# Kernel tuning notes

Measured on AMD Instinct MI355X. Metric: run time of the kernel, lower is better.

## Reference

```python
import jax, jax.numpy as jnp
import numpy as np
from jax.ops import segment_sum

N_NODES = 100000
N_EDGES = 3200000
DIM = 256
N_CLASSES = 32
N_GRAPHS = 64


def setup_inputs() -> dict:
    key = jax.random.key(0)
    k1, k2, k3, k4, k5 = jax.random.split(key, 5)
    x = jax.random.normal(k1, (N_NODES, DIM), dtype=jnp.float32)
    W = jax.random.normal(k2, (DIM, N_CLASSES), dtype=jnp.float32) / np.sqrt(DIM)
    b = jax.random.normal(k3, (N_CLASSES,), dtype=jnp.float32) * 0.01
    edge_index = jax.random.randint(k4, (2, N_EDGES), 0, N_NODES, dtype=jnp.int64)
    batch = jnp.sort(jax.random.randint(k5, (N_NODES,), 0, N_GRAPHS, dtype=jnp.int64))
    return {"x": x, "W": W, "b": b, "edge_index": edge_index, "batch": batch}


def reference(x, W, b, edge_index, batch):
    N = x.shape[0]
    # GCNConv: linear transform (no bias), then normalized aggregation, then bias
    h = x @ W  # [N, C]
    # add self loops (PyG default add_self_loops=True)
    loop = jnp.arange(N, dtype=edge_index.dtype)
    src = jnp.concatenate([edge_index[0], loop])  # source (message sender)
    dst = jnp.concatenate([edge_index[1], loop])  # target (aggregation site)
    # symmetric normalization: deg computed at target with unit edge weights
    deg = segment_sum(jnp.ones_like(dst, dtype=h.dtype), dst, num_segments=N)
    dinv = jnp.where(deg > 0, jax.lax.rsqrt(deg), 0.0)
    norm = dinv[src] * dinv[dst]  # [E+N]
    msg = h[src] * norm[:, None]  # gather + scale
    out = segment_sum(msg, dst, num_segments=N) + b  # scatter-add, bias after agg
    # global_mean_pool: segment mean over graphs
    cnt = segment_sum(jnp.ones((N,), dtype=out.dtype), batch, num_segments=N_GRAPHS)
    sums = segment_sum(out, batch, num_segments=N_GRAPHS)
    return sums / jnp.maximum(cnt, 1.0)[:, None]
```

## Files before the change

kernel.cpp:

```cpp
#include <hip/hip_runtime.h>

#define NN    100000
#define NE    3200000
#define DIMK  256
#define NC    32
#define NG    64

#define ROWS   64
#define NBUCK  1563
#define CAP    2432
#define NB1    512
#define EPB    6250
#define NSL    16
#define MAXG   512

static constexpr size_t OFF_REC    = 0;
static constexpr size_t OFF_DINV   = 15204864;
static constexpr size_t OFF_BTOT   = 15604864;
static constexpr size_t OFF_START  = 15613056;
static constexpr size_t OFF_CTRL   = 15613568;
static constexpr size_t OFF_P2     = 15613696;
static constexpr size_t OFF_PART   = 16662272;
static constexpr size_t OFF_NODEI  = OFF_PART;
static constexpr size_t OFF_CNT    = OFF_PART + 400000;
static constexpr size_t OFF_EXC    = OFF_PART + 3601024;

__device__ __forceinline__ int idx_at(const void* p, long i, bool i64) {
    return i64 ? (int)((const long long*)p)[i] : ((const int*)p)[i];
}

__device__ __forceinline__ bool detect_i64(const void* ei) {
    const int* w = (const int*)ei;
    return (w[1] == 0) & (w[3] == 0) & (w[5] == 0) &
           (w[7] == 0) & (w[9] == 0) & (w[11] == 0);
}

__global__ __launch_bounds__(256) void k_pre(const void* __restrict__ ei,
        unsigned int* __restrict__ parts, int* __restrict__ cnt) {
    __shared__ unsigned int h[12500];
    const bool i64 = detect_i64(ei);
    const int b = blockIdx.x;
    if (b < 256) {
        const int hh = b >> 7;
        const int sl = b & 127;
        const int lo = hh * 50000, hi = lo + 50000;
        for (int t = threadIdx.x; t < 12500; t += 256) h[t] = 0u;
        __syncthreads();
        const int e0 = sl * 25000;
        for (int e = e0 + threadIdx.x; e < e0 + 25000; e += 256) {
            int d = idx_at(ei, (long)NE + e, i64);
            if (d >= lo && d < hi) {
                int r = d - lo;
                atomicAdd(&h[r >> 2], 1u << ((r & 3) * 8));
            }
        }
        __syncthreads();
        for (int t = threadIdx.x; t < 12500; t += 256)
            parts[(size_t)b * 12500 + t] = h[t];
    } else {
        const int k = b - 256;
        for (int t = threadIdx.x; t < NBUCK; t += 256) h[t] = 0u;
        __syncthreads();
        const int e0 = k * EPB;
        for (int e = e0 + threadIdx.x; e < e0 + EPB; e += 256) {
            int s = idx_at(ei, e, i64);
            atomicAdd(&h[s >> 6], 1u);
        }
        __syncthreads();
        for (int t = threadIdx.x; t < NBUCK; t += 256)
            cnt[t * NB1 + k] = (int)h[t];
    }
}

__global__ __launch_bounds__(512) void k_mid(const unsigned int* __restrict__ parts,
        unsigned int* __restrict__ nodeinfo, float* __restrict__ dinv,
        const void* __restrict__ batch, const void* __restrict__ ei,
        int* __restrict__ start, const int* __restrict__ cnt,
        int* __restrict__ exc, int* __restrict__ btot) {
    __shared__ int s[512];
    const int b = blockIdx.x;
    const int t = threadIdx.x;
    if (b < 49) {
        const bool i64 = detect_i64(ei);
        int i = b * 512 + t;
        if (i >= 25000) return;
        int h = (i >= 12500) ? 1 : 0;
        int w = i - h * 12500;
        int c0 = 0, c1 = 0, c2 = 0, c3 = 0;
        const unsigned int* base = parts + (size_t)(h * 128) * 12500 + w;
#pragma unroll 4
        for (int q = 0; q < 128; ++q) {
            unsigned int v = base[(size_t)q * 12500];
            c0 += v & 255u; c1 += (v >> 8) & 255u; c2 += (v >> 16) & 255u; c3 += v >> 24;
        }
        int node = h * 50000 + w * 4;
        dinv[node]     = 1.0f / sqrtf((float)(1 + c0));
        dinv[node + 1] = 1.0f / sqrtf((float)(1 + c1));
        dinv[node + 2] = 1.0f / sqrtf((float)(1 + c2));
        dinv[node + 3] = 1.0f / sqrtf((float)(1 + c3));
        nodeinfo[node]     = ((unsigned)(1 + c0) << 6) | (unsigned)idx_at(batch, node, i64);
        nodeinfo[node + 1] = ((unsigned)(1 + c1) << 6) | (unsigned)idx_at(batch, node + 1, i64);
        nodeinfo[node + 2] = ((unsigned)(1 + c2) << 6) | (unsigned)idx_at(batch, node + 2, i64);
        nodeinfo[node + 3] = ((unsigned)(1 + c3) << 6) | (unsigned)idx_at(batch, node + 3, i64);
    } else if (b < 245) {
        const bool i64 = detect_i64(ei);
        int i = (b - 49) * 512 + t;
        if (i >= NN) return;
        int bi = idx_at(batch, i, i64);
        int bp = (i == 0) ? -1 : idx_at(batch, i - 1, i64);
        for (int g = bp + 1; g <= bi; ++g) start[g] = i;
        if (i == NN - 1)
            for (int g = bi + 1; g <= NG; ++g) start[g] = NN;
    } else {
        const int bkt = b - 245;
        int v = cnt[bkt * NB1 + t];
        s[t] = v;
        __syncthreads();
        for (int off = 1; off < 512; off <<= 1) {
            int u = (t >= off) ? s[t - off] : 0;
            __syncthreads();
            s[t] += u;
            __syncthreads();
        }
        exc[bkt * NB1 + t] = bkt * CAP + (s[t] - v);
        if (t == 511) btot[bkt] = s[511];
    }
}

__global__ __launch_bounds__(256) void k_place(const void* __restrict__ ei,
        const unsigned int* __restrict__ nodeinfo,
        const int* __restrict__ exc, unsigned int* __restrict__ rec,
        int* __restrict__ ctrl) {
    __shared__ unsigned int lc[NBUCK];
    __shared__ int lbase[NBUCK];
    const bool i64 = detect_i64(ei);
    const int k = blockIdx.x;
    if (k == 0 && threadIdx.x == 0) ctrl[1] = 0;
    for (int t = threadIdx.x; t < NBUCK; t += 256) {
        lc[t] = 0u;
        lbase[t] = exc[t * NB1 + k];
    }
    __syncthreads();
    const int e0 = k * EPB;
    for (int e = e0 + threadIdx.x; e < e0 + EPB; e += 256) {
        int s = idx_at(ei, e, i64);
        int d = idx_at(ei, (long)NE + e, i64);
        unsigned int ni = nodeinfo[d];
        unsigned int deg = min(ni >> 6, 1048575u);
        unsigned int g = ni & 63u;
        int b = s >> 6;
        unsigned int r = atomicAdd(&lc[b], 1u);
        rec[lbase[b] + (int)r] = (deg << 12) | (g * 64 + (unsigned)(s & 63));
    }
}

__global__ __launch_bounds__(512, 2) void k_fused(
        const float* __restrict__ x, const float* __restrict__ dinv,
        const void* __restrict__ batch, const void* __restrict__ ei,
        const unsigned int* __restrict__ rec, const int* __restrict__ btot,
        float* __restrict__ part, int* __restrict__ ctrl) {
    __shared__ __align__(16) float Ach[64 * ROWS];
    __shared__ int sbkt;
    const bool i64 = detect_i64(ei);
    const int tid  = threadIdx.x;
    const int gi   = tid >> 6;
    const int lane = tid & 63;

    float acc[8][4];
#pragma unroll
    for (int g = 0; g < 8; ++g)
#pragma unroll
        for (int d = 0; d < 4; ++d) acc[g][d] = 0.0f;

    const float4* x4 = (const float4*)x;
    float4* Ach4 = (float4*)Ach;
    const float4 z4 = make_float4(0.f, 0.f, 0.f, 0.f);
    const int jmax = NN - 1;

    for (;;) {
        if (tid == 0) sbkt = atomicAdd(&ctrl[1], 1);
        __syncthreads();
        const int bkt = sbkt;
        if (bkt >= NBUCK) break;
        const int j0 = bkt * ROWS;

        Ach4[tid] = z4;
        Ach4[tid + 512] = z4;
        __syncthreads();
        if (tid < ROWS) {
            int j = j0 + tid;
            if (j < NN) Ach[idx_at(batch, j, i64) * 64 + tid] = dinv[j];
        }
        __syncthreads();
        {
            const int rb = bkt * CAP;
            const int re = rb + btot[bkt];
            for (int r = rb + tid; r < re; r += 512) {
                unsigned int q = rec[r];
                float val = 1.0f / sqrtf((float)(q >> 12));
                atomicAdd(&Ach[q & 4095u], val);
            }
        }
        __syncthreads();
        float areg[8];
        {
            float dv = dinv[min(j0 + lane, jmax)];
#pragma unroll
            for (int q = 0; q < 8; ++q)
                areg[q] = Ach[(gi * 8 + q) * 64 + lane] * dv;
        }
        __syncthreads();

        if (bkt < NBUCK - 1) {
            const float4* xp = x4 + (size_t)j0 * 64 + lane;
            float4 buf[8];
#pragma unroll
            for (int k = 0; k < 8; ++k) buf[k] = xp[k * 64];
            xp += 512;
            for (int c = 0; c < 8; ++c) {
#pragma unroll
                for (int jj = 0; jj < 8; ++jj) {
                    float4 xv = buf[jj];
                    buf[jj] = xp[jj * 64];
#pragma unroll
                    for (int q = 0; q < 8; ++q) {
                        float aq = __int_as_float(__builtin_amdgcn_readlane(
                            __float_as_int(areg[q]), c * 8 + jj));
                        acc[q][0] = fmaf(aq, xv.x, acc[q][0]);
                        acc[q][1] = fmaf(aq, xv.y, acc[q][1]);
                        acc[q][2] = fmaf(aq, xv.z, acc[q][2]);
                        acc[q][3] = fmaf(aq, xv.w, acc[q][3]);
                    }
                }
                xp += 512;
            }
        } else {
            float4 xv = x4[(size_t)min(j0, jmax) * 64 + lane];
#pragma unroll 4
            for (int jj = 0; jj < ROWS; ++jj) {
                float4 xn = x4[(size_t)min(j0 + jj + 1, jmax) * 64 + lane];
#pragma unroll
                for (int q = 0; q < 8; ++q) {
                    float aq = __int_as_float(__builtin_amdgcn_readlane(
                        __float_as_int(areg[q]), jj));
                    acc[q][0] = fmaf(aq, xv.x, acc[q][0]);
                    acc[q][1] = fmaf(aq, xv.y, acc[q][1]);
                    acc[q][2] = fmaf(aq, xv.z, acc[q][2]);
                    acc[q][3] = fmaf(aq, xv.w, acc[q][3]);
                }
                xv = xn;
            }
        }
    }

    float* p = part + (size_t)blockIdx.x * (NG * DIMK);
#pragma unroll
    for (int g = 0; g < 8; ++g) {
        float4 w = make_float4(acc[g][0], acc[g][1], acc[g][2], acc[g][3]);
        ((float4*)(p + (gi * 8 + g) * DIMK))[lane] = w;
    }
}

__global__ __launch_bounds__(256) void k_reduce1(const float4* __restrict__ part,
        float4* __restrict__ p2, int nblk) {
    int id = blockIdx.x * 256 + threadIdx.x;
    int c4 = id & 4095;
    int sl = id >> 12;
    int span = (nblk + NSL - 1) / NSL;
    int b0 = sl * span, b1 = min(b0 + span, nblk);
    float4 s = make_float4(0.f, 0.f, 0.f, 0.f);
    for (int b = b0; b < b1; ++b) {
        float4 v = part[(size_t)b * 4096 + c4];
        s.x += v.x; s.y += v.y; s.z += v.z; s.w += v.w;
    }
    p2[(size_t)sl * 4096 + c4] = s;
}

__global__ __launch_bounds__(256) void k_final(const float* __restrict__ p2,
        const float* __restrict__ W, const float* __restrict__ bias,
        const int* __restrict__ start, float* __restrict__ out) {
    __shared__ float Sb[8 * DIMK];
    const int tid = threadIdx.x, b = blockIdx.x;
    for (int t = tid; t < 8 * DIMK; t += 256) {
        int gl = t >> 8, d = t & 255;
        float s = 0.f;
#pragma unroll
        for (int sl = 0; sl < NSL; ++sl)
            s += p2[(size_t)sl * (NG * DIMK) + (b * 8 + gl) * DIMK + d];
        Sb[t] = s;
    }
    __syncthreads();
    int g = tid >> 5, c = tid & 31;
    float sum = 0.f;
#pragma unroll 8
    for (int d = 0; d < DIMK; ++d)
        sum = fmaf(Sb[g * DIMK + d], W[d * NC + c], sum);
    int gg = b * 8 + g;
    float cn = (float)max(start[gg + 1] - start[gg], 1);
    out[gg * NC + c] = sum / cn + bias[c];
}

extern "C" void kernel_launch(void* const* d_in, const int* in_sizes, int n_in,
                              void* d_out, int out_size, void* d_ws, size_t ws_size,
                              hipStream_t stream) {
    const float* x    = (const float*)d_in[0];
    const float* W    = (const float*)d_in[1];
    const float* bias = (const float*)d_in[2];
    const void*  ei   = d_in[3];
    const void*  batch= d_in[4];
    float* out = (float*)d_out;

    char* ws = (char*)d_ws;
    unsigned int* rec  = (unsigned int*)(ws + OFF_REC);
    unsigned int* degp = (unsigned int*)(ws + OFF_REC);
    float* dinv  = (float*)(ws + OFF_DINV);
    int*   btot  = (int*)(ws + OFF_BTOT);
    int*   start = (int*)(ws + OFF_START);
    int*   ctrl  = (int*)(ws + OFF_CTRL);
    float* p2    = (float*)(ws + OFF_P2);
    float* part  = (float*)(ws + OFF_PART);
    unsigned int* nodeinfo = (unsigned int*)(ws + OFF_NODEI);
    int*   cnt   = (int*)(ws + OFF_CNT);
    int*   exc   = (int*)(ws + OFF_EXC);

    long avail = (long)(ws_size - OFF_PART) / 65536;
    int grid = (int)avail;
    if (grid > MAXG) grid = MAXG;
    if (grid < 64) grid = 64;

    k_pre    <<<768, 256, 0, stream>>>(ei, degp, cnt);
    k_mid    <<<1808, 512, 0, stream>>>(degp, nodeinfo, dinv, batch, ei, start,
                                        cnt, exc, btot);
    k_place  <<<NB1, 256, 0, stream>>>(ei, nodeinfo, exc, rec, ctrl);
    k_fused  <<<grid, 512, 0, stream>>>(x, dinv, batch, ei, rec, btot, part, ctrl);
    k_reduce1<<<256, 256, 0, stream>>>((const float4*)part, (float4*)p2, grid);
    k_final  <<<8, 256, 0, stream>>>(p2, W, bias, start, out);
}
```

Measured before the change: 199.6 us.

## Split fused aggregation across two feature halves with separate bucket queues

The fused kernel now splits the 256-wide feature dimension into two halves. Even and odd blocks each claim buckets from their own atomic counter and process 128 features with float2 loads, and the grid cap is doubled. Each block holds half the accumulators and writes half-size partials, and the reduce kernel is reindexed to interleave the two halves. This doubles parallelism and cuts register pressure per block, but every bucket's scatter into shared memory (reading rec and doing the atomics) is now repeated by both halves.

New measurement: 215.2 us. +7.8%, slower.

```diff
diff --git a/kernel.cpp b/kernel.cpp
--- a/kernel.cpp
+++ b/kernel.cpp
@@ -12,7 +12,7 @@
 #define NB1    512
 #define EPB    6250
 #define NSL    16
-#define MAXG   512
+#define MAXG   1024
 
 static constexpr size_t OFF_REC    = 0;
 static constexpr size_t OFF_DINV   = 15204864;
@@ -135,7 +135,7 @@
     __shared__ int lbase[NBUCK];
     const bool i64 = detect_i64(ei);
     const int k = blockIdx.x;
-    if (k == 0 && threadIdx.x == 0) ctrl[1] = 0;
+    if (k == 0 && threadIdx.x < 2) ctrl[1 + threadIdx.x] = 0;
     for (int t = threadIdx.x; t < NBUCK; t += 256) {
         lc[t] = 0u;
         lbase[t] = exc[t * NB1 + k];
@@ -165,20 +165,22 @@
     const int tid  = threadIdx.x;
     const int gi   = tid >> 6;
     const int lane = tid & 63;
-
-    float acc[8][4];
-#pragma unroll
-    for (int g = 0; g < 8; ++g)
-#pragma unroll
-        for (int d = 0; d < 4; ++d) acc[g][d] = 0.0f;
-
-    const float4* x4 = (const float4*)x;
+    const int h    = blockIdx.x & 1;
+
+    float acc[8][2];
+#pragma unroll
+    for (int g = 0; g < 8; ++g) {
+        acc[g][0] = 0.0f; acc[g][1] = 0.0f;
+    }
+
+    const float2* x2 = (const float2*)x;
+    const int fcol = h * 64 + lane;
     float4* Ach4 = (float4*)Ach;
     const float4 z4 = make_float4(0.f, 0.f, 0.f, 0.f);
     const int jmax = NN - 1;
 
     for (;;) {
-        if (tid == 0) sbkt = atomicAdd(&ctrl[1], 1);
+        if (tid == 0) sbkt = atomicAdd(&ctrl[1 + h], 1);
         __syncthreads();
         const int bkt = sbkt;
         if (bkt >= NBUCK) break;
@@ -212,53 +214,47 @@
         __syncthreads();
 
         if (bkt < NBUCK - 1) {
-            const float4* xp = x4 + (size_t)j0 * 64 + lane;
-            float4 buf[8];
-#pragma unroll
-            for (int k = 0; k < 8; ++k) buf[k] = xp[k * 64];
-            xp += 512;
+            const float2* xp = x2 + (size_t)j0 * 128 + fcol;
+            float2 buf[8];
+#pragma unroll
+            for (int k = 0; k < 8; ++k) buf[k] = xp[k * 128];
+            xp += 1024;
             for (int c = 0; c < 8; ++c) {
 #pragma unroll
                 for (int jj = 0; jj < 8; ++jj) {
-                    float4 xv = buf[jj];
-                    buf[jj] = xp[jj * 64];
+                    float2 xv = buf[jj];
+                    buf[jj] = xp[jj * 128];
 #pragma unroll
                     for (int q = 0; q < 8; ++q) {
                         float aq = __int_as_float(__builtin_amdgcn_readlane(
                             __float_as_int(areg[q]), c * 8 + jj));
                         acc[q][0] = fmaf(aq, xv.x, acc[q][0]);
                         acc[q][1] = fmaf(aq, xv.y, acc[q][1]);
-                        acc[q][2] = fmaf(aq, xv.z, acc[q][2]);
-                        acc[q][3] = fmaf(aq, xv.w, acc[q][3]);
                     }
                 }
-                xp += 512;
+                xp += 1024;
             }
         } else {
-            float4 xv = x4[(size_t)min(j0, jmax) * 64 + lane];
+            float2 xv = x2[(size_t)min(j0, jmax) * 128 + fcol];
 #pragma unroll 4
             for (int jj = 0; jj < ROWS; ++jj) {
-                float4 xn = x4[(size_t)min(j0 + jj + 1, jmax) * 64 + lane];
+                float2 xn = x2[(size_t)min(j0 + jj + 1, jmax) * 128 + fcol];
 #pragma unroll
                 for (int q = 0; q < 8; ++q) {
                     float aq = __int_as_float(__builtin_amdgcn_readlane(
                         __float_as_int(areg[q]), jj));
                     acc[q][0] = fmaf(aq, xv.x, acc[q][0]);
                     acc[q][1] = fmaf(aq, xv.y, acc[q][1]);
-                    acc[q][2] = fmaf(aq, xv.z, acc[q][2]);
-                    acc[q][3] = fmaf(aq, xv.w, acc[q][3]);
                 }
                 xv = xn;
             }
         }
     }
 
-    float* p = part + (size_t)blockIdx.x * (NG * DIMK);
-#pragma unroll
-    for (int g = 0; g < 8; ++g) {
-        float4 w = make_float4(acc[g][0], acc[g][1], acc[g][2], acc[g][3]);
-        ((float4*)(p + (gi * 8 + g) * DIMK))[lane] = w;
-    }
+    float2* p = (float2*)(part + (size_t)blockIdx.x * (NG * 128));
+#pragma unroll
+    for (int g = 0; g < 8; ++g)
+        p[(gi * 8 + g) * 64 + lane] = make_float2(acc[g][0], acc[g][1]);
 }
 
 __global__ __launch_bounds__(256) void k_reduce1(const float4* __restrict__ part,
@@ -266,11 +262,16 @@
     int id = blockIdx.x * 256 + threadIdx.x;
     int c4 = id & 4095;
     int sl = id >> 12;
-    int span = (nblk + NSL - 1) / NSL;
-    int b0 = sl * span, b1 = min(b0 + span, nblk);
+    int g  = c4 >> 6;
+    int f4 = c4 & 63;
+    int h  = f4 >> 5;
+    int fl = f4 & 31;
+    int nq = (nblk - h + 1) >> 1;
+    int span = (nq + NSL - 1) / NSL;
+    int k0 = sl * span, k1 = min(k0 + span, nq);
     float4 s = make_float4(0.f, 0.f, 0.f, 0.f);
-    for (int b = b0; b < b1; ++b) {
-        float4 v = part[(size_t)b * 4096 + c4];
+    for (int k = k0; k < k1; ++k) {
+        float4 v = part[(size_t)(h + 2 * k) * 2048 + g * 32 + fl];
         s.x += v.x; s.y += v.y; s.z += v.z; s.w += v.w;
     }
     p2[(size_t)sl * 4096 + c4] = s;
@@ -323,9 +324,10 @@
     int*   cnt   = (int*)(ws + OFF_CNT);
     int*   exc   = (int*)(ws + OFF_EXC);
 
-    long avail = (long)(ws_size - OFF_PART) / 65536;
+    long avail = (long)(ws_size - OFF_PART) / 32768;
     int grid = (int)avail;
     if (grid > MAXG) grid = MAXG;
+    grid &= ~1;
     if (grid < 64) grid = 64;
 
     k_pre    <<<768, 256, 0, stream>>>(ei, degp, cnt);
```
